# Kernel optimization log

Hardware: AMD Instinct MI355X
Metric: run time of the kernel (lower is better)

Reference implementation:

```python
import jax, jax.numpy as jnp
from jax import lax
import numpy as np

B, T, H, K = 32, 512, 2048, 128


def setup_inputs() -> dict:
    key = jax.random.key(0)
    k1, k2, k3, k4, k5, k6, k7 = jax.random.split(key, 7)
    hiddens = jax.random.normal(k1, (B, T, H), dtype=jnp.float32)
    mask = jnp.ones((B, T), dtype=jnp.int32)  # mask[:,0] must be on (torchcrf)
    labels = jax.random.randint(k2, (B, T), 0, K)
    W = jax.random.normal(k3, (H, K), dtype=jnp.float32) * 0.02
    b = jnp.zeros((K,), dtype=jnp.float32)
    # torchcrf inits transitions uniform(-0.1, 0.1)
    start_transitions = jax.random.uniform(k4, (K,), minval=-0.1, maxval=0.1)
    end_transitions = jax.random.uniform(k5, (K,), minval=-0.1, maxval=0.1)
    transitions = jax.random.uniform(k6, (K, K), minval=-0.1, maxval=0.1)
    return {"hiddens": hiddens, "mask": mask, "labels": labels, "W": W, "b": b,
            "start_transitions": start_transitions, "end_transitions": end_transitions,
            "transitions": transitions}


def _crf_log_likelihood(emissions, tags, mask, start_t, end_t, trans):
    # emissions: [B,T,K], tags/mask: [B,T]
    Bn, Tn, Kn = emissions.shape
    maskf = mask.astype(emissions.dtype)
    # ---- numerator: score of the gold path ----
    score = start_t[tags[:, 0]] + emissions[jnp.arange(Bn), 0, tags[:, 0]]
    prev, cur = tags[:, :-1], tags[:, 1:]
    emit_cur = jnp.take_along_axis(emissions[:, 1:], cur[..., None], axis=-1)[..., 0]
    score = score + jnp.sum((trans[prev, cur] + emit_cur) * maskf[:, 1:], axis=1)
    last_idx = mask.sum(axis=1).astype(jnp.int32) - 1
    last_tags = jnp.take_along_axis(tags, last_idx[:, None], axis=1)[:, 0]
    score = score + end_t[last_tags]
    # ---- denominator: log partition via stable logsumexp scan ----
    def step(alpha, inp):
        emit_t, m_t = inp  # [B,K], [B]
        nxt = jax.nn.logsumexp(alpha[:, :, None] + trans[None] + emit_t[:, None, :], axis=1)
        alpha = jnp.where(m_t[:, None] > 0, nxt, alpha)
        return alpha, None
    alpha0 = start_t[None, :] + emissions[:, 0]
    emits = jnp.swapaxes(emissions[:, 1:], 0, 1)  # [T-1,B,K]
    ms = jnp.swapaxes(mask[:, 1:], 0, 1)          # [T-1,B]
    alpha, _ = lax.scan(step, alpha0, (emits, ms))
    logZ = jax.nn.logsumexp(alpha + end_t[None, :], axis=1)
    return score - logZ


def _viterbi_decode(emissions, mask, start_t, end_t, trans):
    Bn, Tn, Kn = emissions.shape
    tag_ids = jnp.arange(Kn, dtype=jnp.int32)
    def step(score, inp):
        emit_t, m_t = inp
        cand = score[:, :, None] + trans[None]          # [B,K,K] prev->cur
        bp = jnp.argmax(cand, axis=1).astype(jnp.int32)  # [B,K]
        best = jnp.max(cand, axis=1) + emit_t
        on = m_t[:, None] > 0
        new_score = jnp.where(on, best, score)
        bp = jnp.where(on, bp, tag_ids[None, :])  # identity for padded steps
        return new_score, bp
    score0 = start_t[None, :] + emissions[:, 0]
    emits = jnp.swapaxes(emissions[:, 1:], 0, 1)
    ms = jnp.swapaxes(mask[:, 1:], 0, 1)
    score, history = lax.scan(step, score0, (emits, ms))  # history: [T-1,B,K]
    last_tag = jnp.argmax(score + end_t[None, :], axis=1).astype(jnp.int32)  # [B]
    def back(tag, bp_t):
        tag = jnp.take_along_axis(bp_t, tag[:, None], axis=1)[:, 0]
        return tag, tag
    _, tags_prev = lax.scan(back, last_tag, history, reverse=True)  # [T-1,B]
    tags = jnp.concatenate([tags_prev, last_tag[None, :]], axis=0)  # [T,B]
    return jnp.swapaxes(tags, 0, 1)  # [B,T]


def reference(hiddens, mask, labels, W, b, start_transitions, end_transitions, transitions):
    logits = jnp.einsum('bth,hk->btk', hiddens, W) + b  # emission projection
    decode = _viterbi_decode(logits, mask, start_transitions, end_transitions, transitions)
    llh = _crf_log_likelihood(logits, labels, mask, start_transitions, end_transitions, transitions)
    loss = -jnp.mean(llh)  # -1 * crf(..., reduction='mean')
    return (decode, loss)
```

## Files before the change

### kernel.cpp

```cpp
#include <hip/hip_runtime.h>
#include <hip/hip_bf16.h>
#include <math.h>

#define BB 32
#define TT 512
#define HH 2048
#define KK 128

__global__ __launch_bounds__(256) void gemm_k(const float* __restrict__ hid,
                                              const float* __restrict__ Wm,
                                              const float* __restrict__ bias,
                                              float* __restrict__ logits,
                                              float* __restrict__ loss_slot) {
    constexpr int HC = 16;
    __shared__ float As[HC][68];
    __shared__ float Bs[HC][132];
    const int tid = threadIdx.x;
    const int bid = blockIdx.x;
    if (bid == 0 && tid == 0) loss_slot[0] = 0.0f;
    const int rowBase = bid * 64;
    const int tx = tid & 15, ty = tid >> 4;
    const int ldr = tid >> 2, ldc = tid & 3;
    const int wr = tid >> 4, wc = tid & 15;

    float acc[4][8];
#pragma unroll
    for (int i = 0; i < 4; i++)
#pragma unroll
        for (int j = 0; j < 8; j++) acc[i][j] = 0.0f;

    for (int h0 = 0; h0 < HH; h0 += HC) {
        float4 av = *(const float4*)(hid + (size_t)(rowBase + ldr) * HH + h0 + ldc * 4);
        float4 bv0 = *(const float4*)(Wm + (size_t)(h0 + wr) * KK + wc * 8);
        float4 bv1 = *(const float4*)(Wm + (size_t)(h0 + wr) * KK + wc * 8 + 4);
        __syncthreads();
        As[ldc * 4 + 0][ldr] = av.x;
        As[ldc * 4 + 1][ldr] = av.y;
        As[ldc * 4 + 2][ldr] = av.z;
        As[ldc * 4 + 3][ldr] = av.w;
        *(float4*)&Bs[wr][wc * 8] = bv0;
        *(float4*)&Bs[wr][wc * 8 + 4] = bv1;
        __syncthreads();
#pragma unroll
        for (int h = 0; h < HC; ++h) {
            float4 a = *(const float4*)&As[h][ty * 4];
            float4 b0 = *(const float4*)&Bs[h][tx * 4];
            float4 b1 = *(const float4*)&Bs[h][tx * 4 + 64];
            float ar[4] = {a.x, a.y, a.z, a.w};
            float br[8] = {b0.x, b0.y, b0.z, b0.w, b1.x, b1.y, b1.z, b1.w};
#pragma unroll
            for (int i = 0; i < 4; i++)
#pragma unroll
                for (int j = 0; j < 8; j++) acc[i][j] = fmaf(ar[i], br[j], acc[i][j]);
        }
    }
    float bb[8];
    {
        float4 b0v = *(const float4*)(bias + tx * 4);
        float4 b1v = *(const float4*)(bias + tx * 4 + 64);
        bb[0] = b0v.x; bb[1] = b0v.y; bb[2] = b0v.z; bb[3] = b0v.w;
        bb[4] = b1v.x; bb[5] = b1v.y; bb[6] = b1v.z; bb[7] = b1v.w;
    }
#pragma unroll
    for (int i = 0; i < 4; i++) {
        int row = rowBase + ty * 4 + i;
        float4 o0 = make_float4(acc[i][0] + bb[0], acc[i][1] + bb[1], acc[i][2] + bb[2], acc[i][3] + bb[3]);
        float4 o1 = make_float4(acc[i][4] + bb[4], acc[i][5] + bb[5], acc[i][6] + bb[6], acc[i][7] + bb[7]);
        *(float4*)(logits + (size_t)row * KK + tx * 4) = o0;
        *(float4*)(logits + (size_t)row * KK + tx * 4 + 64) = o1;
    }
}

struct SMemB {
    float ubuf[2][144];
    int mbuf[512];
    float red[4];
    int redi[4];
    float vbuf[128];
};

__global__ __launch_bounds__(256) void scan_k(const float* __restrict__ logits,
                                              const int* __restrict__ mask,
                                              const int* __restrict__ labels,
                                              const float* __restrict__ startT,
                                              const float* __restrict__ endT,
                                              const float* __restrict__ trans,
                                              float* __restrict__ shist,
                                              float* __restrict__ out) {
    __shared__ SMemB sm;
    const int tid = threadIdx.x;
    const int bid = blockIdx.x;
    const float L2E = 1.4426950408889634f;
    const int s = tid & 3;
    const int jb = tid >> 2;
    const int j0 = jb * 2;
    const int padw = j0 + 4 * (j0 >> 5);

    if (bid < BB) {
        const int b = bid;
        const float* lrow = logits + (size_t)b * TT * KK;
        float V0[32], V1[32];
#pragma unroll
        for (int k = 0; k < 32; k++) {
            V0[k] = exp2f(trans[(s * 32 + k) * KK + j0] * L2E);
            V1[k] = exp2f(trans[(s * 32 + k) * KK + j0 + 1] * L2E);
        }
        sm.mbuf[tid] = mask[b * TT + tid];
        sm.mbuf[tid + 256] = mask[b * TT + 256 + tid];
        float a0_ = (startT[j0] + lrow[j0]) * L2E;
        float a1_ = (startT[j0 + 1] + lrow[j0 + 1]) * L2E;
        float off = (startT[0] + lrow[0]) * L2E;
        if (s == 0) {
            sm.ubuf[0][padw] = exp2f(a0_ - off);
            sm.ubuf[0][padw + 1] = exp2f(a1_ - off);
        }
        __syncthreads();
        int cur = 0;
        float2 em_next = *(const float2*)(lrow + KK + j0);
        for (int t = 1; t < TT; ++t) {
            float2 em = em_next;
            if (t + 1 < TT) em_next = *(const float2*)(lrow + (size_t)(t + 1) * KK + j0);
            if (sm.mbuf[t]) {
                const float* ub = &sm.ubuf[cur][s * 36];
                float u00 = sm.ubuf[cur][0];
                float uu[32];
#pragma unroll
                for (int c = 0; c < 8; ++c) {
                    float4 v = *(const float4*)(ub + c * 4);
                    uu[c * 4] = v.x; uu[c * 4 + 1] = v.y; uu[c * 4 + 2] = v.z; uu[c * 4 + 3] = v.w;
                }
                float p0e = 0.f, p0o = 0.f, p1e = 0.f, p1o = 0.f;
#pragma unroll
                for (int k = 0; k < 32; k += 2) {
                    p0e = fmaf(uu[k], V0[k], p0e);
                    p1e = fmaf(uu[k], V1[k], p1e);
                    p0o = fmaf(uu[k + 1], V0[k + 1], p0o);
                    p1o = fmaf(uu[k + 1], V1[k + 1], p1o);
                }
                float w0 = p0e + p0o, w1 = p1e + p1o;
                w0 += __shfl_xor(w0, 1, 64);
                w0 += __shfl_xor(w0, 2, 64);
                w1 += __shfl_xor(w1, 1, 64);
                w1 += __shfl_xor(w1, 2, 64);
                a0_ = log2f(w0) + off + em.x * L2E;
                a1_ = log2f(w1) + off + em.y * L2E;
                float offn = off + log2f(u00);
                if (s == 0) {
                    sm.ubuf[cur ^ 1][padw] = exp2f(a0_ - offn);
                    sm.ubuf[cur ^ 1][padw + 1] = exp2f(a1_ - offn);
                }
                off = offn;
                cur ^= 1;
                __syncthreads();
            }
        }
        if (s == 0) {
            sm.vbuf[j0] = a0_ + endT[j0] * L2E;
            sm.vbuf[j0 + 1] = a1_ + endT[j0 + 1] * L2E;
        }
        __syncthreads();

        float part = 0.0f;
        int cnt = 0;
        for (int tt = tid; tt < TT; tt += 256) {
            int mv = sm.mbuf[tt];
            cnt += mv;
            if (tt == 0) {
                int l0 = labels[b * TT];
                part += startT[l0] + lrow[l0];
            } else if (mv) {
                int lc = labels[b * TT + tt];
                int lp = labels[b * TT + tt - 1];
                part += trans[lp * KK + lc] + lrow[(size_t)tt * KK + lc];
            }
        }
#pragma unroll
        for (int d = 1; d < 64; d <<= 1) {
            part += __shfl_xor(part, d, 64);
            cnt += __shfl_xor(cnt, d, 64);
        }
        int wid = tid >> 6, lane = tid & 63;
        if (lane == 0) { sm.red[wid] = part; sm.redi[wid] = cnt; }
        __syncthreads();
        if (tid == 0) {
            float score = 0.0f;
            int total = 0;
            for (int i = 0; i < 4; i++) { score += sm.red[i]; total += sm.redi[i]; }
            score += endT[labels[b * TT + total - 1]];
            float mx = -3.0e38f;
            for (int i = 0; i < 128; i++) mx = fmaxf(mx, sm.vbuf[i]);
            float ssum = 0.0f;
            for (int i = 0; i < 128; i++) ssum += exp2f(sm.vbuf[i] - mx);
            float logZ = (mx + log2f(ssum)) * 0.6931471805599453f;
            float llh = score - logZ;
            atomicAdd(out + BB * TT, -llh * (1.0f / 32.0f));
        }
    } else {
        const int b = bid - BB;
        const float* lrow = logits + (size_t)b * TT * KK;
        float* hist = shist + (size_t)b * TT * KK;
        float T0[32], T1[32];
#pragma unroll
        for (int k = 0; k < 32; k++) {
            T0[k] = trans[(s * 32 + k) * KK + j0];
            T1[k] = trans[(s * 32 + k) * KK + j0 + 1];
        }
        sm.mbuf[tid] = mask[b * TT + tid];
        sm.mbuf[tid + 256] = mask[b * TT + 256 + tid];
        float s0_ = startT[j0] + lrow[j0];
        float s1_ = startT[j0 + 1] + lrow[j0 + 1];
        if (s == 0) {
            sm.ubuf[0][padw] = s0_;
            sm.ubuf[0][padw + 1] = s1_;
        } else if (s == 1) {
            *(float2*)(hist + j0) = make_float2(s0_, s1_);
        }
        __syncthreads();
        int cur = 0;
        float2 em_next = *(const float2*)(lrow + KK + j0);
        for (int t = 1; t < TT; ++t) {
            float2 em = em_next;
            if (t + 1 < TT) em_next = *(const float2*)(lrow + (size_t)(t + 1) * KK + j0);
            if (sm.mbuf[t]) {
                const float* ub = &sm.ubuf[cur][s * 36];
                float uu[32];
#pragma unroll
                for (int c = 0; c < 8; ++c) {
                    float4 v = *(const float4*)(ub + c * 4);
                    uu[c * 4] = v.x; uu[c * 4 + 1] = v.y; uu[c * 4 + 2] = v.z; uu[c * 4 + 3] = v.w;
                }
                float m0 = -3.0e38f, m1 = -3.0e38f;
#pragma unroll
                for (int k = 0; k < 32; k += 2) {
                    m0 = fmaxf(m0, fmaxf(uu[k] + T0[k], uu[k + 1] + T0[k + 1]));
                    m1 = fmaxf(m1, fmaxf(uu[k] + T1[k], uu[k + 1] + T1[k + 1]));
                }
                m0 = fmaxf(m0, __shfl_xor(m0, 1, 64));
                m0 = fmaxf(m0, __shfl_xor(m0, 2, 64));
                m1 = fmaxf(m1, __shfl_xor(m1, 1, 64));
                m1 = fmaxf(m1, __shfl_xor(m1, 2, 64));
                s0_ = m0 + em.x;
                s1_ = m1 + em.y;
                if (s == 0) {
                    sm.ubuf[cur ^ 1][padw] = s0_;
                    sm.ubuf[cur ^ 1][padw + 1] = s1_;
                } else if (s == 1) {
                    *(float2*)(hist + (size_t)t * KK + j0) = make_float2(s0_, s1_);
                }
                cur ^= 1;
                __syncthreads();
            } else {
                if (s == 1) *(float2*)(hist + (size_t)t * KK + j0) = make_float2(s0_, s1_);
            }
        }
    }
}

__global__ __launch_bounds__(256) void bp_k(const float* __restrict__ shist,
                                            const float* __restrict__ trans,
                                            const int* __restrict__ mask,
                                            unsigned char* __restrict__ bp) {
    const int t = blockIdx.x + 1;
    const int tid = threadIdx.x;
    const int j = tid & 127, bg = tid >> 7;
    __shared__ float sc[BB][KK];
    for (int i = tid; i < BB * KK; i += 256) {
        int bb2 = i >> 7;
        sc[bb2][i & 127] = shist[(size_t)bb2 * TT * KK + (size_t)(t - 1) * KK + (i & 127)];
    }
    __syncthreads();
    float m[16];
    int idx[16];
#pragma unroll
    for (int c = 0; c < 16; c++) { m[c] = -3.0e38f; idx[c] = 0; }
#pragma unroll 4
    for (int i = 0; i < 128; ++i) {
        float tr = trans[i * KK + j];
#pragma unroll
        for (int c = 0; c < 16; c++) {
            float cand = sc[bg + 2 * c][i] + tr;
            if (cand > m[c]) { m[c] = cand; idx[c] = i; }
        }
    }
#pragma unroll
    for (int c = 0; c < 16; c++) {
        int bb2 = bg + 2 * c;
        int v = idx[c];
        if (mask[bb2 * TT + t] == 0) v = j;
        bp[(size_t)bb2 * TT * KK + (size_t)t * KK + j] = (unsigned char)v;
    }
}

__global__ __launch_bounds__(512) void bt_k(const float* __restrict__ shist,
                                            const float* __restrict__ endT,
                                            const unsigned char* __restrict__ bp,
                                            float* __restrict__ out) {
    const int b = blockIdx.x;
    const int tid = threadIdx.x;
    const int lane = tid & 63, w = tid >> 6;
    __shared__ float cb[128];
    __shared__ int tagbuf[512];
    __shared__ int handoff;
    if (tid < 128) cb[tid] = shist[(size_t)b * TT * KK + (size_t)(TT - 1) * KK + tid] + endT[tid];
    __syncthreads();
    if (tid == 0) {
        float mm = cb[0];
        int bi = 0;
        for (int i = 1; i < 128; i++)
            if (cb[i] > mm) { mm = cb[i]; bi = i; }
        tagbuf[TT - 1] = bi;
        handoff = bi;
    }
    unsigned int reg[64];
    const unsigned char* bpb = bp + (size_t)b * TT * KK;
#pragma unroll
    for (int r = 0; r < 64; r++) {
        int t_row = w * 64 + 1 + r;
        unsigned int v = 0;
        if (t_row < TT) v = *(const unsigned short*)(bpb + (size_t)t_row * KK + lane * 2);
        reg[r] = v;
    }
    __syncthreads();
    for (int ph = 7; ph >= 0; --ph) {
        if (w == ph) {
            int tag = handoff;
#pragma unroll
            for (int r = 63; r >= 0; --r) {
                int t_row = ph * 64 + 1 + r;
                if (t_row < TT) {
                    unsigned int vv = (unsigned int)__shfl((int)reg[r], tag >> 1, 64);
                    tag = (int)((vv >> ((tag & 1) * 8)) & 0xffu);
                    if (lane == 0) tagbuf[t_row - 1] = tag;
                }
            }
            if (lane == 0) handoff = tag;
        }
        __syncthreads();
    }
    out[b * TT + tid] = (float)tagbuf[tid];
}

extern "C" void kernel_launch(void* const* d_in, const int* in_sizes, int n_in,
                              void* d_out, int out_size, void* d_ws, size_t ws_size,
                              hipStream_t stream) {
    const float* hid = (const float*)d_in[0];
    const int* mask = (const int*)d_in[1];
    const int* labels = (const int*)d_in[2];
    const float* Wm = (const float*)d_in[3];
    const float* bias = (const float*)d_in[4];
    const float* startT = (const float*)d_in[5];
    const float* endT = (const float*)d_in[6];
    const float* trans = (const float*)d_in[7];
    float* out = (float*)d_out;
    char* ws = (char*)d_ws;

    float* logits = (float*)ws;
    float* shist = (float*)(ws + 8388608);
    unsigned char* bp = (unsigned char*)(ws + 16777216);

    gemm_k<<<256, 256, 0, stream>>>(hid, Wm, bias, logits, out + BB * TT);
    scan_k<<<64, 256, 0, stream>>>(logits, mask, labels, startT, endT, trans, shist, out);
    bp_k<<<TT - 1, 256, 0, stream>>>(shist, trans, mask, bp);
    bt_k<<<BB, 512, 0, stream>>>(shist, endT, bp, out);
}
```

Before: 708.3 us.

## Split-K GEMM with 512 threads, exp-domain forward scan, ballot masks, vectorized backpointer

The emission GEMM now splits the hidden dimension across four thread groups, each computing an 8x8 register tile, and reduces their partial sums through shared memory. The goal is more in-flight work per block. The forward CRF scan stays in the exp domain: it rescales by the reciprocal of the first element and accumulates the log offset, which removes per-step log/exp pairs from the serial chain. Per-step shared-memory mask lookups are replaced with ballot bitmasks. The backpointer kernel now uses float4 loads and a 4-way unrolled argmax. The risks are extra reductions and syncs in the GEMM, and possible exp-domain underflow or overflow in the scan.

Result: faster. 685.8 us (-3.2%).

```diff
diff --git a/kernel.cpp b/kernel.cpp
--- a/kernel.cpp
+++ b/kernel.cpp
@@ -7,73 +7,107 @@
 #define HH 2048
 #define KK 128
 
-__global__ __launch_bounds__(256) void gemm_k(const float* __restrict__ hid,
+__global__ __launch_bounds__(512) void gemm_k(const float* __restrict__ hid,
                                               const float* __restrict__ Wm,
                                               const float* __restrict__ bias,
                                               float* __restrict__ logits,
                                               float* __restrict__ loss_slot) {
-    constexpr int HC = 16;
-    __shared__ float As[HC][68];
-    __shared__ float Bs[HC][132];
-    const int tid = threadIdx.x;
-    const int bid = blockIdx.x;
+    __shared__ union {
+        struct { float As[4][16][72]; float Bs[4][16][132]; } s;
+        float4 red[16][128];
+    } sm;
+    const int tid = threadIdx.x, bid = blockIdx.x;
     if (bid == 0 && tid == 0) loss_slot[0] = 0.0f;
+    const int g = tid >> 7, lt = tid & 127;
     const int rowBase = bid * 64;
-    const int tx = tid & 15, ty = tid >> 4;
-    const int ldr = tid >> 2, ldc = tid & 3;
-    const int wr = tid >> 4, wc = tid & 15;
-
-    float acc[4][8];
-#pragma unroll
-    for (int i = 0; i < 4; i++)
+    const int rowg = lt >> 4, colg = lt & 15;
+    const int arow = lt >> 1, ahq = lt & 1;
+
+    float acc[8][8];
+#pragma unroll
+    for (int i = 0; i < 8; i++)
 #pragma unroll
         for (int j = 0; j < 8; j++) acc[i][j] = 0.0f;
 
-    for (int h0 = 0; h0 < HH; h0 += HC) {
-        float4 av = *(const float4*)(hid + (size_t)(rowBase + ldr) * HH + h0 + ldc * 4);
-        float4 bv0 = *(const float4*)(Wm + (size_t)(h0 + wr) * KK + wc * 8);
-        float4 bv1 = *(const float4*)(Wm + (size_t)(h0 + wr) * KK + wc * 8 + 4);
-        __syncthreads();
-        As[ldc * 4 + 0][ldr] = av.x;
-        As[ldc * 4 + 1][ldr] = av.y;
-        As[ldc * 4 + 2][ldr] = av.z;
-        As[ldc * 4 + 3][ldr] = av.w;
-        *(float4*)&Bs[wr][wc * 8] = bv0;
-        *(float4*)&Bs[wr][wc * 8 + 4] = bv1;
-        __syncthreads();
-#pragma unroll
-        for (int h = 0; h < HC; ++h) {
-            float4 a = *(const float4*)&As[h][ty * 4];
-            float4 b0 = *(const float4*)&Bs[h][tx * 4];
-            float4 b1 = *(const float4*)&Bs[h][tx * 4 + 64];
-            float ar[4] = {a.x, a.y, a.z, a.w};
+    const float* hA = hid + (size_t)(rowBase + arow) * HH + g * 512 + ahq * 8;
+
+    for (int it = 0; it < 32; ++it) {
+        const int h0 = g * 512 + it * 16;
+        float4 a0 = *(const float4*)(hA + it * 16);
+        float4 a1 = *(const float4*)(hA + it * 16 + 4);
+        float4 bv[4];
+#pragma unroll
+        for (int r = 0; r < 4; ++r) {
+            int idx = r * 128 + lt;
+            bv[r] = *(const float4*)(Wm + (size_t)(h0 + (idx >> 5)) * KK + (idx & 31) * 4);
+        }
+        __syncthreads();
+        const int hb = ahq * 8;
+        sm.s.As[g][hb + 0][arow] = a0.x;
+        sm.s.As[g][hb + 1][arow] = a0.y;
+        sm.s.As[g][hb + 2][arow] = a0.z;
+        sm.s.As[g][hb + 3][arow] = a0.w;
+        sm.s.As[g][hb + 4][arow] = a1.x;
+        sm.s.As[g][hb + 5][arow] = a1.y;
+        sm.s.As[g][hb + 6][arow] = a1.z;
+        sm.s.As[g][hb + 7][arow] = a1.w;
+#pragma unroll
+        for (int r = 0; r < 4; ++r) {
+            int idx = r * 128 + lt;
+            *(float4*)&sm.s.Bs[g][idx >> 5][(idx & 31) * 4] = bv[r];
+        }
+        __syncthreads();
+#pragma unroll
+        for (int h = 0; h < 16; ++h) {
+            float4 aL = *(const float4*)&sm.s.As[g][h][rowg * 8];
+            float4 aH = *(const float4*)&sm.s.As[g][h][rowg * 8 + 4];
+            float4 b0 = *(const float4*)&sm.s.Bs[g][h][colg * 4];
+            float4 b1 = *(const float4*)&sm.s.Bs[g][h][64 + colg * 4];
+            float ar[8] = {aL.x, aL.y, aL.z, aL.w, aH.x, aH.y, aH.z, aH.w};
             float br[8] = {b0.x, b0.y, b0.z, b0.w, b1.x, b1.y, b1.z, b1.w};
 #pragma unroll
-            for (int i = 0; i < 4; i++)
+            for (int i = 0; i < 8; i++)
 #pragma unroll
                 for (int j = 0; j < 8; j++) acc[i][j] = fmaf(ar[i], br[j], acc[i][j]);
         }
     }
-    float bb[8];
-    {
-        float4 b0v = *(const float4*)(bias + tx * 4);
-        float4 b1v = *(const float4*)(bias + tx * 4 + 64);
-        bb[0] = b0v.x; bb[1] = b0v.y; bb[2] = b0v.z; bb[3] = b0v.w;
-        bb[4] = b1v.x; bb[5] = b1v.y; bb[6] = b1v.z; bb[7] = b1v.w;
-    }
-#pragma unroll
-    for (int i = 0; i < 4; i++) {
-        int row = rowBase + ty * 4 + i;
-        float4 o0 = make_float4(acc[i][0] + bb[0], acc[i][1] + bb[1], acc[i][2] + bb[2], acc[i][3] + bb[3]);
-        float4 o1 = make_float4(acc[i][4] + bb[4], acc[i][5] + bb[5], acc[i][6] + bb[6], acc[i][7] + bb[7]);
-        *(float4*)(logits + (size_t)row * KK + tx * 4) = o0;
-        *(float4*)(logits + (size_t)row * KK + tx * 4 + 64) = o1;
+    __syncthreads();
+    for (int gp = 1; gp <= 3; ++gp) {
+        if (g == gp) {
+#pragma unroll
+            for (int i = 0; i < 8; ++i) {
+                sm.red[i * 2][lt] = make_float4(acc[i][0], acc[i][1], acc[i][2], acc[i][3]);
+                sm.red[i * 2 + 1][lt] = make_float4(acc[i][4], acc[i][5], acc[i][6], acc[i][7]);
+            }
+        }
+        __syncthreads();
+        if (g == 0) {
+#pragma unroll
+            for (int i = 0; i < 8; ++i) {
+                float4 r0 = sm.red[i * 2][lt];
+                float4 r1 = sm.red[i * 2 + 1][lt];
+                acc[i][0] += r0.x; acc[i][1] += r0.y; acc[i][2] += r0.z; acc[i][3] += r0.w;
+                acc[i][4] += r1.x; acc[i][5] += r1.y; acc[i][6] += r1.z; acc[i][7] += r1.w;
+            }
+        }
+        __syncthreads();
+    }
+    if (g == 0) {
+        float4 bb0 = *(const float4*)(bias + colg * 4);
+        float4 bb1 = *(const float4*)(bias + 64 + colg * 4);
+#pragma unroll
+        for (int i = 0; i < 8; ++i) {
+            int row = rowBase + rowg * 8 + i;
+            *(float4*)(logits + (size_t)row * KK + colg * 4) =
+                make_float4(acc[i][0] + bb0.x, acc[i][1] + bb0.y, acc[i][2] + bb0.z, acc[i][3] + bb0.w);
+            *(float4*)(logits + (size_t)row * KK + 64 + colg * 4) =
+                make_float4(acc[i][4] + bb1.x, acc[i][5] + bb1.y, acc[i][6] + bb1.z, acc[i][7] + bb1.w);
+        }
     }
 }
 
 struct SMemB {
     float ubuf[2][144];
-    int mbuf[512];
     float red[4];
     int redi[4];
     float vbuf[128];
@@ -95,24 +129,28 @@
     const int jb = tid >> 2;
     const int j0 = jb * 2;
     const int padw = j0 + 4 * (j0 >> 5);
+    const int lane = tid & 63;
 
     if (bid < BB) {
         const int b = bid;
         const float* lrow = logits + (size_t)b * TT * KK;
+        unsigned long long mb[8];
+#pragma unroll
+        for (int c = 0; c < 8; ++c) mb[c] = __ballot(mask[b * TT + c * 64 + lane]);
         float V0[32], V1[32];
 #pragma unroll
         for (int k = 0; k < 32; k++) {
             V0[k] = exp2f(trans[(s * 32 + k) * KK + j0] * L2E);
             V1[k] = exp2f(trans[(s * 32 + k) * KK + j0 + 1] * L2E);
         }
-        sm.mbuf[tid] = mask[b * TT + tid];
-        sm.mbuf[tid + 256] = mask[b * TT + 256 + tid];
         float a0_ = (startT[j0] + lrow[j0]) * L2E;
         float a1_ = (startT[j0 + 1] + lrow[j0 + 1]) * L2E;
-        float off = (startT[0] + lrow[0]) * L2E;
+        float OFF = (startT[0] + lrow[0]) * L2E;
+        float S0_ = exp2f(a0_ - OFF);
+        float S1_ = exp2f(a1_ - OFF);
         if (s == 0) {
-            sm.ubuf[0][padw] = exp2f(a0_ - off);
-            sm.ubuf[0][padw + 1] = exp2f(a1_ - off);
+            sm.ubuf[0][padw] = S0_;
+            sm.ubuf[0][padw + 1] = S1_;
         }
         __syncthreads();
         int cur = 0;
@@ -120,7 +158,8 @@
         for (int t = 1; t < TT; ++t) {
             float2 em = em_next;
             if (t + 1 < TT) em_next = *(const float2*)(lrow + (size_t)(t + 1) * KK + j0);
-            if (sm.mbuf[t]) {
+            int mt = (int)((mb[t >> 6] >> (t & 63)) & 1ull);
+            if (mt) {
                 const float* ub = &sm.ubuf[cur][s * 36];
                 float u00 = sm.ubuf[cur][0];
                 float uu[32];
@@ -129,6 +168,10 @@
                     float4 v = *(const float4*)(ub + c * 4);
                     uu[c * 4] = v.x; uu[c * 4 + 1] = v.y; uu[c * 4 + 2] = v.z; uu[c * 4 + 3] = v.w;
                 }
+                float r00 = __builtin_amdgcn_rcpf(u00);
+                float sc0 = exp2f(em.x * L2E) * r00;
+                float sc1 = exp2f(em.y * L2E) * r00;
+                OFF += log2f(u00);
                 float p0e = 0.f, p0o = 0.f, p1e = 0.f, p1o = 0.f;
 #pragma unroll
                 for (int k = 0; k < 32; k += 2) {
@@ -142,71 +185,70 @@
                 w0 += __shfl_xor(w0, 2, 64);
                 w1 += __shfl_xor(w1, 1, 64);
                 w1 += __shfl_xor(w1, 2, 64);
-                a0_ = log2f(w0) + off + em.x * L2E;
-                a1_ = log2f(w1) + off + em.y * L2E;
-                float offn = off + log2f(u00);
+                S0_ = w0 * sc0;
+                S1_ = w1 * sc1;
                 if (s == 0) {
-                    sm.ubuf[cur ^ 1][padw] = exp2f(a0_ - offn);
-                    sm.ubuf[cur ^ 1][padw + 1] = exp2f(a1_ - offn);
-                }
-                off = offn;
+                    sm.ubuf[cur ^ 1][padw] = S0_;
+                    sm.ubuf[cur ^ 1][padw + 1] = S1_;
+                }
                 cur ^= 1;
-                __syncthreads();
-            }
+            }
+            __syncthreads();
         }
         if (s == 0) {
-            sm.vbuf[j0] = a0_ + endT[j0] * L2E;
-            sm.vbuf[j0 + 1] = a1_ + endT[j0 + 1] * L2E;
+            sm.vbuf[j0] = log2f(S0_) + endT[j0] * L2E;
+            sm.vbuf[j0 + 1] = log2f(S1_) + endT[j0 + 1] * L2E;
         }
         __syncthreads();
 
         float part = 0.0f;
-        int cnt = 0;
         for (int tt = tid; tt < TT; tt += 256) {
-            int mv = sm.mbuf[tt];
-            cnt += mv;
             if (tt == 0) {
                 int l0 = labels[b * TT];
                 part += startT[l0] + lrow[l0];
-            } else if (mv) {
+            } else if (mask[b * TT + tt]) {
                 int lc = labels[b * TT + tt];
                 int lp = labels[b * TT + tt - 1];
                 part += trans[lp * KK + lc] + lrow[(size_t)tt * KK + lc];
             }
         }
 #pragma unroll
-        for (int d = 1; d < 64; d <<= 1) {
-            part += __shfl_xor(part, d, 64);
-            cnt += __shfl_xor(cnt, d, 64);
-        }
-        int wid = tid >> 6, lane = tid & 63;
-        if (lane == 0) { sm.red[wid] = part; sm.redi[wid] = cnt; }
-        __syncthreads();
-        if (tid == 0) {
-            float score = 0.0f;
-            int total = 0;
-            for (int i = 0; i < 4; i++) { score += sm.red[i]; total += sm.redi[i]; }
-            score += endT[labels[b * TT + total - 1]];
-            float mx = -3.0e38f;
-            for (int i = 0; i < 128; i++) mx = fmaxf(mx, sm.vbuf[i]);
-            float ssum = 0.0f;
-            for (int i = 0; i < 128; i++) ssum += exp2f(sm.vbuf[i] - mx);
-            float logZ = (mx + log2f(ssum)) * 0.6931471805599453f;
-            float llh = score - logZ;
-            atomicAdd(out + BB * TT, -llh * (1.0f / 32.0f));
+        for (int d = 1; d < 64; d <<= 1) part += __shfl_xor(part, d, 64);
+        int wid = tid >> 6;
+        if (lane == 0) sm.red[wid] = part;
+        __syncthreads();
+        if (tid < 64) {
+            float v0 = sm.vbuf[tid], v1 = sm.vbuf[tid + 64];
+            float mx = fmaxf(v0, v1);
+#pragma unroll
+            for (int d = 1; d < 64; d <<= 1) mx = fmaxf(mx, __shfl_xor(mx, d, 64));
+            float p = exp2f(v0 - mx) + exp2f(v1 - mx);
+#pragma unroll
+            for (int d = 1; d < 64; d <<= 1) p += __shfl_xor(p, d, 64);
+            if (tid == 0) {
+                int total = 0;
+#pragma unroll
+                for (int c = 0; c < 8; ++c) total += __popcll(mb[c]);
+                float score = sm.red[0] + sm.red[1] + sm.red[2] + sm.red[3];
+                score += endT[labels[b * TT + total - 1]];
+                float logZ = (OFF + mx + log2f(p)) * 0.6931471805599453f;
+                float llh = score - logZ;
+                atomicAdd(out + BB * TT, -llh * (1.0f / 32.0f));
+            }
         }
     } else {
         const int b = bid - BB;
         const float* lrow = logits + (size_t)b * TT * KK;
         float* hist = shist + (size_t)b * TT * KK;
+        unsigned long long mb[8];
+#pragma unroll
+        for (int c = 0; c < 8; ++c) mb[c] = __ballot(mask[b * TT + c * 64 + lane]);
         float T0[32], T1[32];
 #pragma unroll
         for (int k = 0; k < 32; k++) {
             T0[k] = trans[(s * 32 + k) * KK + j0];
             T1[k] = trans[(s * 32 + k) * KK + j0 + 1];
         }
-        sm.mbuf[tid] = mask[b * TT + tid];
-        sm.mbuf[tid + 256] = mask[b * TT + 256 + tid];
         float s0_ = startT[j0] + lrow[j0];
         float s1_ = startT[j0 + 1] + lrow[j0 + 1];
         if (s == 0) {
@@ -221,7 +263,8 @@
         for (int t = 1; t < TT; ++t) {
             float2 em = em_next;
             if (t + 1 < TT) em_next = *(const float2*)(lrow + (size_t)(t + 1) * KK + j0);
-            if (sm.mbuf[t]) {
+            int mt = (int)((mb[t >> 6] >> (t & 63)) & 1ull);
+            if (mt) {
                 const float* ub = &sm.ubuf[cur][s * 36];
                 float uu[32];
 #pragma unroll
@@ -248,10 +291,10 @@
                     *(float2*)(hist + (size_t)t * KK + j0) = make_float2(s0_, s1_);
                 }
                 cur ^= 1;
-                __syncthreads();
             } else {
                 if (s == 1) *(float2*)(hist + (size_t)t * KK + j0) = make_float2(s0_, s1_);
             }
+            __syncthreads();
         }
     }
 }
@@ -264,22 +307,31 @@
     const int tid = threadIdx.x;
     const int j = tid & 127, bg = tid >> 7;
     __shared__ float sc[BB][KK];
-    for (int i = tid; i < BB * KK; i += 256) {
-        int bb2 = i >> 7;
-        sc[bb2][i & 127] = shist[(size_t)bb2 * TT * KK + (size_t)(t - 1) * KK + (i & 127)];
+#pragma unroll
+    for (int r = 0; r < 4; ++r) {
+        int f = tid + r * 256;
+        int bb2 = f >> 5, c4 = (f & 31) * 4;
+        *(float4*)&sc[bb2][c4] = *(const float4*)&shist[(size_t)bb2 * TT * KK + (size_t)(t - 1) * KK + c4];
     }
     __syncthreads();
     float m[16];
     int idx[16];
 #pragma unroll
     for (int c = 0; c < 16; c++) { m[c] = -3.0e38f; idx[c] = 0; }
-#pragma unroll 4
-    for (int i = 0; i < 128; ++i) {
-        float tr = trans[i * KK + j];
+    for (int i4 = 0; i4 < 32; ++i4) {
+        const int ib = i4 * 4;
+        float tr0 = trans[(ib + 0) * KK + j];
+        float tr1 = trans[(ib + 1) * KK + j];
+        float tr2 = trans[(ib + 2) * KK + j];
+        float tr3 = trans[(ib + 3) * KK + j];
 #pragma unroll
         for (int c = 0; c < 16; c++) {
-            float cand = sc[bg + 2 * c][i] + tr;
-            if (cand > m[c]) { m[c] = cand; idx[c] = i; }
+            float4 s4 = *(const float4*)&sc[bg + 2 * c][ib];
+            float c0 = s4.x + tr0, c1 = s4.y + tr1, c2 = s4.z + tr2, c3 = s4.w + tr3;
+            if (c0 > m[c]) { m[c] = c0; idx[c] = ib; }
+            if (c1 > m[c]) { m[c] = c1; idx[c] = ib + 1; }
+            if (c2 > m[c]) { m[c] = c2; idx[c] = ib + 2; }
+            if (c3 > m[c]) { m[c] = c3; idx[c] = ib + 3; }
         }
     }
 #pragma unroll
@@ -358,7 +410,7 @@
     float* shist = (float*)(ws + 8388608);
     unsigned char* bp = (unsigned char*)(ws + 16777216);
 
-    gemm_k<<<256, 256, 0, stream>>>(hid, Wm, bias, logits, out + BB * TT);
+    gemm_k<<<256, 512, 0, stream>>>(hid, Wm, bias, logits, out + BB * TT);
     scan_k<<<64, 256, 0, stream>>>(logits, mask, labels, startT, endT, trans, shist, out);
     bp_k<<<TT - 1, 256, 0, stream>>>(shist, trans, mask, bp);
     bt_k<<<BB, 512, 0, stream>>>(shist, endT, bp, out);
```
